# Kernel optimization log

Hardware: AMD Instinct MI355X
Metric: run time of the kernel (lower is better)

The kernel has to match this reference:

```python
import jax, jax.numpy as jnp
import numpy as np

N_VOX = 500000
P, S, K = 2048, 64, 8          # pixels(rays), samples per ray, voxel neighbors per sample
F_M, F_H = 64, 128             # voxel feature dim, mlp hidden dim
FREQ_PE = 4
DEPTH_MIN, DEPTH_MAX = 1.0, 80.0
RAY_SAMPLE_STEPS = 64.0
EPS = 1e-10
IN_FEAT = F_M + 3 * FREQ_PE * 2  # 88


def lrelu(x):
    return jnp.where(x >= 0, x, 0.1 * x)  # LeakyReLU(0.1)


def posenc(x, L=FREQ_PE):
    # NeRF positional encoding: sin/cos(2^i * x), i in [0, L)
    freqs = 2.0 ** jnp.arange(L, dtype=x.dtype)          # [L]
    ang = x[..., None] * freqs                            # [..., 3, L]
    enc = jnp.concatenate([jnp.sin(ang), jnp.cos(ang)], axis=-1)  # [..., 3, 2L]
    return enc.reshape(x.shape[:-1] + (x.shape[-1] * 2 * L,))


def setup_inputs() -> dict:
    key = jax.random.key(0)
    ks = jax.random.split(key, 16)

    def xavier(k, fan_in, fan_out):
        return jax.random.normal(k, (fan_in, fan_out), jnp.float32) / np.sqrt(fan_in)

    inp = {
        'map_xyz': jax.random.normal(ks[0], (N_VOX, 3), jnp.float32),
        'map_feat': jax.random.normal(ks[1], (N_VOX, F_M), jnp.float32) * 0.05,
        'ind_voxel': jax.random.randint(ks[2], (P, S, K), 0, N_VOX),
        'sample_xyz': jax.random.normal(ks[3], (P, S, 3), jnp.float32),
        'dist_to_cam': jax.random.uniform(ks[4], (P, S), jnp.float32) * RAY_SAMPLE_STEPS,
        'W0': xavier(ks[5], IN_FEAT, F_H), 'b0': jnp.full((F_H,), 0.01, jnp.float32),
        'W1': xavier(ks[6], F_H, F_H),     'b1': jnp.full((F_H,), 0.01, jnp.float32),
        'W2': xavier(ks[7], F_H, F_H),     'b2': jnp.full((F_H,), 0.01, jnp.float32),
        'Wa0': xavier(ks[8], F_H, F_H // 2), 'ba0': jnp.full((F_H // 2,), 0.01, jnp.float32),
        'Wa1': xavier(ks[9], F_H // 2, 1),   'ba1': jnp.full((1,), 0.01, jnp.float32),
        'Wr0': xavier(ks[10], F_H, F_H // 2), 'br0': jnp.full((F_H // 2,), 0.01, jnp.float32),
        'Wr1': xavier(ks[11], F_H // 2, 3),   'br1': jnp.full((3,), 0.01, jnp.float32),
    }
    return inp


def reference(map_xyz, map_feat, ind_voxel, sample_xyz, dist_to_cam,
              W0, b0, W1, b1, W2, b2, Wa0, ba0, Wa1, ba1, Wr0, br0, Wr1, br1):
    # ---- voxel -> sample messages (func_msg_voxel_to_sample) ----
    voxel_xyz = map_xyz[ind_voxel]                       # [P,S,K,3] gather
    feat = map_feat[ind_voxel]                           # [P,S,K,F_M] gather
    offset = sample_xyz[:, :, None, :] - voxel_xyz       # [P,S,K,3]
    h = jnp.concatenate([feat, posenc(offset)], axis=-1) # [P,S,K,88]
    h = lrelu(h @ W0 + b0)
    h = lrelu(h @ W1 + b1)
    h = lrelu(h @ W2 + b2)                               # [P,S,K,F_H]
    w = jnp.exp(-10.0 * jnp.linalg.norm(offset, axis=-1))  # [P,S,K]
    w = w / jnp.sum(w, axis=-1, keepdims=True)
    # ---- reduce over K neighbors (func_reduce_voxel_to_sample) ----
    feat_s = jnp.sum(h * w[..., None], axis=2)           # [P,S,F_H]
    a = lrelu(feat_s @ Wa0 + ba0)
    alpha = jax.nn.sigmoid(a @ Wa1 + ba1)                # [P,S,1]
    r = lrelu(feat_s @ Wr0 + br0)
    rgb = jax.nn.sigmoid(r @ Wr1 + br1)                  # [P,S,3]
    # ---- sample -> pixel volume rendering (func_reduce_sample_to_pixel) ----
    dist = DEPTH_MIN + DEPTH_MAX * dist_to_cam / RAY_SAMPLE_STEPS  # [P,S]
    ones = jnp.ones((P, 1, 1), alpha.dtype)
    trans = jnp.cumprod(jnp.concatenate([ones, 1.0 - alpha + EPS], axis=1), axis=1)[:, :-1, :]
    blend = alpha * trans                                # [P,S,1]
    pixel_rgb = jnp.sum(rgb * blend, axis=1)             # [P,3]
    pixel_d = jnp.sum(dist[..., None] * blend, axis=1)   # [P,1]
    acc = jnp.sum(blend, axis=1)                         # [P,1]
    return jnp.concatenate([pixel_rgb, pixel_d, acc], axis=-1)  # [P,5]
```

## Files before the change

### kernel.cpp

```cpp
#include <hip/hip_runtime.h>

typedef __bf16 bf16_t;
typedef __bf16 bf16x8 __attribute__((ext_vector_type(8)));
typedef float  f32x4  __attribute__((ext_vector_type(4)));

#define NPIX 2048
#define NS   64
#define NK   8
#define NSAMP (NPIX*NS)
#define NROWS (NSAMP*NK)
#define TROWS 64
#define NTILES (NROWS/TROWS)
#define XSTR 104
#define HSTR 136

#define PK_W0 0
#define PK_W1 1536
#define PK_W2 3584
#define PK_WA 5632
#define PK_WR 6656
#define PK_TOT 7680

#define WS_AR_BYTES 122880

__global__ void pack_weights(const float* __restrict__ W0, const float* __restrict__ W1,
                             const float* __restrict__ W2, const float* __restrict__ Wa0,
                             const float* __restrict__ Wr0, bf16_t* __restrict__ dst0) {
  int tid = blockIdx.x * blockDim.x + threadIdx.x;
  if (tid >= PK_TOT * 8) return;
  const float* src; bf16_t* dst; int e, KD, ND, KS;
  if (tid < 12288)      { src = W0;  dst = dst0;         e = tid;         KD = 88;  ND = 128; KS = 3; }
  else if (tid < 28672) { src = W1;  dst = dst0 + 12288; e = tid - 12288; KD = 128; ND = 128; KS = 4; }
  else if (tid < 45056) { src = W2;  dst = dst0 + 28672; e = tid - 28672; KD = 128; ND = 128; KS = 4; }
  else if (tid < 53248) { src = Wa0; dst = dst0 + 45056; e = tid - 45056; KD = 128; ND = 64;  KS = 4; }
  else                  { src = Wr0; dst = dst0 + 53248; e = tid - 53248; KD = 128; ND = 64;  KS = 4; }
  int j = e & 7, l = (e >> 3) & 63, f = e >> 9;
  int s = f % KS, t = f / KS;
  int row = s * 32 + (l >> 4) * 8 + j;
  int col = t * 16 + (l & 15);
  float v = (row < KD) ? src[row * ND + col] : 0.f;
  dst[e] = (bf16_t)v;
}

__global__ __launch_bounds__(512, 4)
void nerf_main(const float* __restrict__ map_xyz, const float* __restrict__ map_feat,
               const int* __restrict__ ind, const float* __restrict__ sample_xyz,
               const float* __restrict__ b0g, const float* __restrict__ b1g,
               const float* __restrict__ b2g, const float* __restrict__ ba0g,
               const float* __restrict__ wa1g, const float* __restrict__ ba1g,
               const float* __restrict__ br0g, const float* __restrict__ wr1g,
               const float* __restrict__ br1g, const bf16_t* __restrict__ wpack,
               float* __restrict__ ar_out)
{
  __shared__ __align__(16) bf16_t sBuf[TROWS * HSTR];
  __shared__ __align__(16) bf16_t sHa[TROWS * HSTR];
  __shared__ __align__(16) bf16_t sFS[16 * HSTR];
  __shared__ float sWt[TROWS];
  __shared__ float sWs[8];
  __shared__ float sA[8 * 68];
  __shared__ float sR[8 * 68];
  __shared__ float sWa1[64];
  __shared__ float sWr1[192];

  const int tid = threadIdx.x;
  const int wid = tid >> 6, l = tid & 63;
  const int q = l >> 4, n = l & 15;

  const bf16x8* pk = (const bf16x8*)wpack;
  bf16x8 w0f[3], w1f[4], w2f[4], hdf[4];
#pragma unroll
  for (int s = 0; s < 3; s++) w0f[s] = pk[PK_W0 + (wid * 3 + s) * 64 + l];
#pragma unroll
  for (int s = 0; s < 4; s++) w1f[s] = pk[PK_W1 + (wid * 4 + s) * 64 + l];
#pragma unroll
  for (int s = 0; s < 4; s++) w2f[s] = pk[PK_W2 + (wid * 4 + s) * 64 + l];
#pragma unroll
  for (int s = 0; s < 4; s++)
    hdf[s] = pk[(wid < 4 ? PK_WA : PK_WR) + ((wid & 3) * 4 + s) * 64 + l];

  const int col = wid * 16 + n;
  const float bias0 = b0g[col], bias1 = b1g[col], bias2 = b2g[col];
  const float biasH = (wid < 4) ? ba0g[(wid & 3) * 16 + n] : br0g[(wid & 3) * 16 + n];

  if (tid < 64) sWa1[tid] = wa1g[tid];
  else if (tid < 256) sWr1[tid - 64] = wr1g[tid - 64];
  for (int i = tid; i < 8 * HSTR; i += 512) sFS[8 * HSTR + i] = (bf16_t)0.f;
  const float ba1v = ba1g[0];
  const float br1v0 = br1g[0], br1v1 = br1g[1], br1v2 = br1g[2];
  __syncthreads();

  for (int tile = blockIdx.x; tile < NTILES; tile += gridDim.x) {
    const int m0 = tile * TROWS;

    {
      int r = tid >> 3, part = tid & 7;
      int idx = ind[m0 + r];
      const float4* fp = (const float4*)(map_feat + (size_t)idx * 64 + part * 8);
      float4 f0 = fp[0], f1 = fp[1];
      bf16x8 v;
      v[0] = (bf16_t)f0.x; v[1] = (bf16_t)f0.y; v[2] = (bf16_t)f0.z; v[3] = (bf16_t)f0.w;
      v[4] = (bf16_t)f1.x; v[5] = (bf16_t)f1.y; v[6] = (bf16_t)f1.z; v[7] = (bf16_t)f1.w;
      *(bf16x8*)(sBuf + r * XSTR + part * 8) = v;
    }
    if (tid < 64) {
      int m = m0 + tid;
      int idx = ind[m];
      int g = m >> 3;
      float ox = sample_xyz[g * 3 + 0] - map_xyz[idx * 3 + 0];
      float oy = sample_xyz[g * 3 + 1] - map_xyz[idx * 3 + 1];
      float oz = sample_xyz[g * 3 + 2] - map_xyz[idx * 3 + 2];
      sWt[tid] = __expf(-10.f * sqrtf(ox * ox + oy * oy + oz * oz));
      float o3[3] = {ox, oy, oz};
      bf16_t* xr = sBuf + tid * XSTR + 64;
#pragma unroll
      for (int d = 0; d < 3; d++) {
        float x = o3[d];
        bf16x8 e;
        float fr = 1.f;
#pragma unroll
        for (int i = 0; i < 4; i++) {
          e[i]     = (bf16_t)__sinf(x * fr);
          e[4 + i] = (bf16_t)__cosf(x * fr);
          fr *= 2.f;
        }
        *(bf16x8*)(xr + d * 8) = e;
      }
      bf16x8 z = {};
      *(bf16x8*)(xr + 24) = z;
    }
    __syncthreads();

    if (tid < 8) {
      float ss = 0.f;
#pragma unroll
      for (int k = 0; k < 8; k++) ss += sWt[tid * 8 + k];
      sWs[tid] = ss;
    }

    {
      f32x4 acc[4] = {};
#pragma unroll
      for (int s = 0; s < 3; s++)
#pragma unroll
        for (int g = 0; g < 4; g++) {
          bf16x8 a = *(const bf16x8*)(sBuf + (g * 16 + n) * XSTR + s * 32 + q * 8);
          acc[g] = __builtin_amdgcn_mfma_f32_16x16x32_bf16(a, w0f[s], acc[g], 0, 0, 0);
        }
#pragma unroll
      for (int g = 0; g < 4; g++)
#pragma unroll
        for (int i = 0; i < 4; i++) {
          float v = acc[g][i] + bias0;
          v = (v >= 0.f) ? v : 0.1f * v;
          sHa[(g * 16 + q * 4 + i) * HSTR + col] = (bf16_t)v;
        }
    }
    __syncthreads();

    auto mlp_layer = [&](const bf16_t* In, bf16_t* Out, bf16x8 (&wf)[4], float bias) {
      f32x4 acc[4] = {};
#pragma unroll
      for (int s = 0; s < 4; s++)
#pragma unroll
        for (int g = 0; g < 4; g++) {
          bf16x8 a = *(const bf16x8*)(In + (g * 16 + n) * HSTR + s * 32 + q * 8);
          acc[g] = __builtin_amdgcn_mfma_f32_16x16x32_bf16(a, wf[s], acc[g], 0, 0, 0);
        }
#pragma unroll
      for (int g = 0; g < 4; g++)
#pragma unroll
        for (int i = 0; i < 4; i++) {
          float v = acc[g][i] + bias;
          v = (v >= 0.f) ? v : 0.1f * v;
          Out[(g * 16 + q * 4 + i) * HSTR + col] = (bf16_t)v;
        }
    };
    mlp_layer(sHa, sBuf, w1f, bias1);
    __syncthreads();
    mlp_layer(sBuf, sHa, w2f, bias2);
    __syncthreads();

    {
      int j = tid >> 6;
      int c = (tid & 63) * 2;
      float a0 = 0.f, a1 = 0.f;
#pragma unroll
      for (int k = 0; k < 8; k++) {
        float wk = sWt[j * 8 + k];
        unsigned u = *(const unsigned*)(sHa + (j * 8 + k) * HSTR + c);
        a0 += wk * __uint_as_float(u << 16);
        a1 += wk * __uint_as_float(u & 0xffff0000u);
      }
      float inv = 1.f / sWs[j];
      sFS[j * HSTR + c]     = (bf16_t)(a0 * inv);
      sFS[j * HSTR + c + 1] = (bf16_t)(a1 * inv);
    }
    __syncthreads();

    {
      f32x4 ha = {};
#pragma unroll
      for (int s = 0; s < 4; s++) {
        bf16x8 a = *(const bf16x8*)(sFS + n * HSTR + s * 32 + q * 8);
        ha = __builtin_amdgcn_mfma_f32_16x16x32_bf16(a, hdf[s], ha, 0, 0, 0);
      }
      if (q < 2) {
        float* dst = (wid < 4) ? sA : sR;
#pragma unroll
        for (int i = 0; i < 4; i++) {
          float v = ha[i] + biasH;
          v = (v >= 0.f) ? v : 0.1f * v;
          dst[(q * 4 + i) * 68 + (wid & 3) * 16 + n] = v;
        }
      }
    }
    __syncthreads();

    if (tid < 8) {
      float x = ba1v;
#pragma unroll
      for (int h = 0; h < 64; h++) x += sA[tid * 68 + h] * sWa1[h];
      float alpha = 1.f / (1.f + __expf(-x));
      ar_out[(size_t)(m0 / 8 + tid) * 4 + 3] = alpha;
    } else if (tid < 32) {
      int j = (tid - 8) / 3, ch = (tid - 8) % 3;
      float x = (ch == 0) ? br1v0 : (ch == 1) ? br1v1 : br1v2;
#pragma unroll
      for (int h = 0; h < 64; h++) x += sR[j * 68 + h] * sWr1[h * 3 + ch];
      float c2 = 1.f / (1.f + __expf(-x));
      ar_out[(size_t)(m0 / 8 + j) * 4 + ch] = c2;
    }
  }
}

__global__ __launch_bounds__(512)
void render_kernel(const float* __restrict__ ar, const float* __restrict__ dcam,
                   float* __restrict__ out) {
  int ray = blockIdx.x * 8 + (threadIdx.x >> 6);
  int s = threadIdx.x & 63;
  float4 v = ((const float4*)ar)[ray * 64 + s];
  float alpha = v.w;
  float t = 1.f - alpha + 1e-10f;
  float p = t;
#pragma unroll
  for (int d = 1; d < 64; d <<= 1) {
    float o = __shfl_up(p, d);
    if (s >= d) p *= o;
  }
  float pm1 = __shfl_up(p, 1);
  float T = (s == 0) ? 1.f : pm1;
  float bl = alpha * T;
  float dist = 1.f + 1.25f * dcam[ray * 64 + s];
  float cr = v.x * bl, cg = v.y * bl, cb = v.z * bl, cd = dist * bl, ca = bl;
#pragma unroll
  for (int d = 32; d > 0; d >>= 1) {
    cr += __shfl_xor(cr, d);
    cg += __shfl_xor(cg, d);
    cb += __shfl_xor(cb, d);
    cd += __shfl_xor(cd, d);
    ca += __shfl_xor(ca, d);
  }
  if (s == 0) {
    out[ray * 5 + 0] = cr; out[ray * 5 + 1] = cg; out[ray * 5 + 2] = cb;
    out[ray * 5 + 3] = cd; out[ray * 5 + 4] = ca;
  }
}

extern "C" void kernel_launch(void* const* d_in, const int* in_sizes, int n_in,
                              void* d_out, int out_size, void* d_ws, size_t ws_size,
                              hipStream_t stream) {
  const float* map_xyz    = (const float*)d_in[0];
  const float* map_feat   = (const float*)d_in[1];
  const int*   ind        = (const int*)d_in[2];
  const float* sample_xyz = (const float*)d_in[3];
  const float* dist_cam   = (const float*)d_in[4];
  const float* W0  = (const float*)d_in[5];
  const float* b0  = (const float*)d_in[6];
  const float* W1  = (const float*)d_in[7];
  const float* b1  = (const float*)d_in[8];
  const float* W2  = (const float*)d_in[9];
  const float* b2  = (const float*)d_in[10];
  const float* Wa0 = (const float*)d_in[11];
  const float* ba0 = (const float*)d_in[12];
  const float* Wa1 = (const float*)d_in[13];
  const float* ba1 = (const float*)d_in[14];
  const float* Wr0 = (const float*)d_in[15];
  const float* br0 = (const float*)d_in[16];
  const float* Wr1 = (const float*)d_in[17];
  const float* br1 = (const float*)d_in[18];

  bf16_t* wpack = (bf16_t*)d_ws;
  float*  ar    = (float*)((char*)d_ws + WS_AR_BYTES);

  pack_weights<<<240, 256, 0, stream>>>(W0, W1, W2, Wa0, Wr0, wpack);
  nerf_main<<<512, 512, 0, stream>>>(map_xyz, map_feat, ind, sample_xyz,
                                     b0, b1, b2, ba0, Wa1, ba1, br0, Wr1, br1,
                                     wpack, ar);
  render_kernel<<<256, 512, 0, stream>>>(ar, dist_cam, (float*)d_out);
}
```

Before: 418.5 us.

## Fuse K-reduction into layer-2 epilogue and parallelize gather, posenc, and heads

The layer-2 MFMA epilogue now applies the per-neighbor weights and reduces over K directly from accumulators using a shuffle, so the separate sHa round-trip and reduction phase go away. Positional encoding is spread across all 512 threads, each computing one sin or cos set with double-angle identities, instead of 64 threads each doing 24 transcendentals. The final alpha and rgb heads become wave-wide shuffle reductions with one float4 store per sample, replacing serial 64-step loops in 32 threads. The double-angle recurrences may lose a little accuracy compared with direct sin and cos.

```diff
diff --git a/kernel.cpp b/kernel.cpp
--- a/kernel.cpp
+++ b/kernel.cpp
@@ -1,6 +1,7 @@
 #include <hip/hip_runtime.h>
 
 typedef __bf16 bf16_t;
+typedef __bf16 bf16x4 __attribute__((ext_vector_type(4)));
 typedef __bf16 bf16x8 __attribute__((ext_vector_type(8)));
 typedef float  f32x4  __attribute__((ext_vector_type(4)));
 
@@ -42,6 +43,9 @@
   dst[e] = (bf16_t)v;
 }
 
+__device__ __forceinline__ float lrelu(float v) { return fmaxf(v, 0.1f * v); }
+__device__ __forceinline__ float sigmoidf(float x) { return 1.f / (1.f + __expf(-x)); }
+
 __global__ __launch_bounds__(512, 4)
 void nerf_main(const float* __restrict__ map_xyz, const float* __restrict__ map_feat,
                const int* __restrict__ ind, const float* __restrict__ sample_xyz,
@@ -55,7 +59,7 @@
   __shared__ __align__(16) bf16_t sBuf[TROWS * HSTR];
   __shared__ __align__(16) bf16_t sHa[TROWS * HSTR];
   __shared__ __align__(16) bf16_t sFS[16 * HSTR];
-  __shared__ float sWt[TROWS];
+  __shared__ __align__(16) float sWt[TROWS];
   __shared__ float sWs[8];
   __shared__ float sA[8 * 68];
   __shared__ float sR[8 * 68];
@@ -93,40 +97,36 @@
     const int m0 = tile * TROWS;
 
     {
-      int r = tid >> 3, part = tid & 7;
-      int idx = ind[m0 + r];
-      const float4* fp = (const float4*)(map_feat + (size_t)idx * 64 + part * 8);
+      const int r = tid >> 3, p = tid & 7;
+      const int m = m0 + r;
+      const int idx = ind[m];
+      const float4* fp = (const float4*)(map_feat + (size_t)idx * 64 + p * 8);
       float4 f0 = fp[0], f1 = fp[1];
       bf16x8 v;
       v[0] = (bf16_t)f0.x; v[1] = (bf16_t)f0.y; v[2] = (bf16_t)f0.z; v[3] = (bf16_t)f0.w;
       v[4] = (bf16_t)f1.x; v[5] = (bf16_t)f1.y; v[6] = (bf16_t)f1.z; v[7] = (bf16_t)f1.w;
-      *(bf16x8*)(sBuf + r * XSTR + part * 8) = v;
-    }
-    if (tid < 64) {
-      int m = m0 + tid;
-      int idx = ind[m];
-      int g = m >> 3;
-      float ox = sample_xyz[g * 3 + 0] - map_xyz[idx * 3 + 0];
-      float oy = sample_xyz[g * 3 + 1] - map_xyz[idx * 3 + 1];
-      float oz = sample_xyz[g * 3 + 2] - map_xyz[idx * 3 + 2];
-      sWt[tid] = __expf(-10.f * sqrtf(ox * ox + oy * oy + oz * oz));
-      float o3[3] = {ox, oy, oz};
-      bf16_t* xr = sBuf + tid * XSTR + 64;
-#pragma unroll
-      for (int d = 0; d < 3; d++) {
-        float x = o3[d];
-        bf16x8 e;
-        float fr = 1.f;
-#pragma unroll
-        for (int i = 0; i < 4; i++) {
-          e[i]     = (bf16_t)__sinf(x * fr);
-          e[4 + i] = (bf16_t)__cosf(x * fr);
-          fr *= 2.f;
-        }
-        *(bf16x8*)(xr + d * 8) = e;
-      }
-      bf16x8 z = {};
-      *(bf16x8*)(xr + 24) = z;
+      *(bf16x8*)(sBuf + r * XSTR + p * 8) = v;
+      const int g = m >> 3;
+      if (p < 6) {
+        const int d = p >> 1;
+        float o = sample_xyz[g * 3 + d] - map_xyz[idx * 3 + d];
+        float s1 = __sinf(o), c1 = __cosf(o);
+        float s2 = 2.f * s1 * c1, c2 = 1.f - 2.f * s1 * s1;
+        float s4 = 2.f * s2 * c2, c4 = 1.f - 2.f * s2 * s2;
+        float s8 = 2.f * s4 * c4, c8 = 1.f - 2.f * s4 * s4;
+        bf16x4 e;
+        if (p & 1) { e[0] = (bf16_t)c1; e[1] = (bf16_t)c2; e[2] = (bf16_t)c4; e[3] = (bf16_t)c8; }
+        else       { e[0] = (bf16_t)s1; e[1] = (bf16_t)s2; e[2] = (bf16_t)s4; e[3] = (bf16_t)s8; }
+        *(bf16x4*)(sBuf + r * XSTR + 64 + d * 8 + (p & 1) * 4) = e;
+      } else if (p == 6) {
+        bf16x8 z = {};
+        *(bf16x8*)(sBuf + r * XSTR + 88) = z;
+      } else {
+        float ox = sample_xyz[g * 3 + 0] - map_xyz[idx * 3 + 0];
+        float oy = sample_xyz[g * 3 + 1] - map_xyz[idx * 3 + 1];
+        float oz = sample_xyz[g * 3 + 2] - map_xyz[idx * 3 + 2];
+        sWt[r] = __expf(-10.f * sqrtf(ox * ox + oy * oy + oz * oz));
+      }
     }
     __syncthreads();
 
@@ -150,50 +150,54 @@
       for (int g = 0; g < 4; g++)
 #pragma unroll
         for (int i = 0; i < 4; i++) {
-          float v = acc[g][i] + bias0;
-          v = (v >= 0.f) ? v : 0.1f * v;
+          float v = lrelu(acc[g][i] + bias0);
           sHa[(g * 16 + q * 4 + i) * HSTR + col] = (bf16_t)v;
         }
     }
     __syncthreads();
 
-    auto mlp_layer = [&](const bf16_t* In, bf16_t* Out, bf16x8 (&wf)[4], float bias) {
+    {
       f32x4 acc[4] = {};
 #pragma unroll
       for (int s = 0; s < 4; s++)
 #pragma unroll
         for (int g = 0; g < 4; g++) {
-          bf16x8 a = *(const bf16x8*)(In + (g * 16 + n) * HSTR + s * 32 + q * 8);
-          acc[g] = __builtin_amdgcn_mfma_f32_16x16x32_bf16(a, wf[s], acc[g], 0, 0, 0);
+          bf16x8 a = *(const bf16x8*)(sHa + (g * 16 + n) * HSTR + s * 32 + q * 8);
+          acc[g] = __builtin_amdgcn_mfma_f32_16x16x32_bf16(a, w1f[s], acc[g], 0, 0, 0);
         }
 #pragma unroll
       for (int g = 0; g < 4; g++)
 #pragma unroll
         for (int i = 0; i < 4; i++) {
-          float v = acc[g][i] + bias;
-          v = (v >= 0.f) ? v : 0.1f * v;
-          Out[(g * 16 + q * 4 + i) * HSTR + col] = (bf16_t)v;
-        }
-    };
-    mlp_layer(sHa, sBuf, w1f, bias1);
-    __syncthreads();
-    mlp_layer(sBuf, sHa, w2f, bias2);
-    __syncthreads();
-
-    {
-      int j = tid >> 6;
-      int c = (tid & 63) * 2;
-      float a0 = 0.f, a1 = 0.f;
-#pragma unroll
-      for (int k = 0; k < 8; k++) {
-        float wk = sWt[j * 8 + k];
-        unsigned u = *(const unsigned*)(sHa + (j * 8 + k) * HSTR + c);
-        a0 += wk * __uint_as_float(u << 16);
-        a1 += wk * __uint_as_float(u & 0xffff0000u);
-      }
-      float inv = 1.f / sWs[j];
-      sFS[j * HSTR + c]     = (bf16_t)(a0 * inv);
-      sFS[j * HSTR + c + 1] = (bf16_t)(a1 * inv);
+          float v = lrelu(acc[g][i] + bias1);
+          sBuf[(g * 16 + q * 4 + i) * HSTR + col] = (bf16_t)v;
+        }
+    }
+    __syncthreads();
+
+    {
+      f32x4 acc[4] = {};
+#pragma unroll
+      for (int s = 0; s < 4; s++)
+#pragma unroll
+        for (int g = 0; g < 4; g++) {
+          bf16x8 a = *(const bf16x8*)(sBuf + (g * 16 + n) * HSTR + s * 32 + q * 8);
+          acc[g] = __builtin_amdgcn_mfma_f32_16x16x32_bf16(a, w2f[s], acc[g], 0, 0, 0);
+        }
+#pragma unroll
+      for (int g = 0; g < 4; g++) {
+        const int j = 2 * g + (q >> 1);
+        const float4 wt4 = *(const float4*)(sWt + j * 8 + 4 * (q & 1));
+        float part = 0.f;
+#pragma unroll
+        for (int i = 0; i < 4; i++) {
+          float v = lrelu(acc[g][i] + bias2);
+          part += ((const float*)&wt4)[i] * v;
+        }
+        part += __shfl_xor(part, 16);
+        float fs = part * __builtin_amdgcn_rcpf(sWs[j]);
+        if (!(q & 1)) sFS[j * HSTR + col] = (bf16_t)fs;
+      }
     }
     __syncthreads();
 
@@ -208,27 +212,35 @@
         float* dst = (wid < 4) ? sA : sR;
 #pragma unroll
         for (int i = 0; i < 4; i++) {
-          float v = ha[i] + biasH;
-          v = (v >= 0.f) ? v : 0.1f * v;
+          float v = lrelu(ha[i] + biasH);
           dst[(q * 4 + i) * 68 + (wid & 3) * 16 + n] = v;
         }
       }
     }
     __syncthreads();
 
-    if (tid < 8) {
-      float x = ba1v;
-#pragma unroll
-      for (int h = 0; h < 64; h++) x += sA[tid * 68 + h] * sWa1[h];
-      float alpha = 1.f / (1.f + __expf(-x));
-      ar_out[(size_t)(m0 / 8 + tid) * 4 + 3] = alpha;
-    } else if (tid < 32) {
-      int j = (tid - 8) / 3, ch = (tid - 8) % 3;
-      float x = (ch == 0) ? br1v0 : (ch == 1) ? br1v1 : br1v2;
-#pragma unroll
-      for (int h = 0; h < 64; h++) x += sR[j * 68 + h] * sWr1[h * 3 + ch];
-      float c2 = 1.f / (1.f + __expf(-x));
-      ar_out[(size_t)(m0 / 8 + j) * 4 + ch] = c2;
+    {
+      float vA = sA[wid * 68 + l];
+      float vR = sR[wid * 68 + l];
+      float xa = vA * sWa1[l];
+      float x0 = vR * sWr1[l * 3 + 0];
+      float x1 = vR * sWr1[l * 3 + 1];
+      float x2 = vR * sWr1[l * 3 + 2];
+#pragma unroll
+      for (int d = 32; d > 0; d >>= 1) {
+        xa += __shfl_xor(xa, d);
+        x0 += __shfl_xor(x0, d);
+        x1 += __shfl_xor(x1, d);
+        x2 += __shfl_xor(x2, d);
+      }
+      if (l == 0) {
+        float4 o;
+        o.x = sigmoidf(x0 + br1v0);
+        o.y = sigmoidf(x1 + br1v1);
+        o.z = sigmoidf(x2 + br1v2);
+        o.w = sigmoidf(xa + ba1v);
+        ((float4*)ar_out)[m0 / 8 + wid] = o;
+      }
     }
   }
 }
```

Measured after the change: 417.1 us. No clear change (-0.3%).
